# Performance work log

Measured on AMD Instinct MI355X. Metric: run time of the kernel, lower is better.

Reference implementation:

```python
import jax, jax.numpy as jnp
import numpy as np


def setup_inputs() -> dict:
    key = jax.random.key(0)
    k1, k2, k3 = jax.random.split(key, 3)
    B, S, H = 16, 4096, 512           # batch, frames, encoder feature dim
    G, V, D = 2, 320, 128             # groups, codevectors/group, group dim
    return {
        "hidden_states": jax.random.normal(k1, (B, S, H), dtype=jnp.float32),
        "W_proj": jax.random.normal(k2, (H, G * D), dtype=jnp.float32) * 0.02,
        "b_proj": jnp.zeros((G * D,), dtype=jnp.float32),
        "codevectors": jax.random.normal(k3, (G, V, D), dtype=jnp.float32),
    }


def reference(hidden_states, W_proj, b_proj, codevectors):
    B, S, _ = hidden_states.shape
    G, V, D = codevectors.shape
    # project to codevector_dim, split into groups: [B,S,G,D]
    h = (hidden_states @ W_proj + b_proj).reshape(B, S, G, D)
    # squared L2 distances per group, via ||h||^2 - 2 h.c + ||c||^2 -> [G,B,S,V]
    hc = jnp.einsum('bsgd,gvd->gbsv', h, codevectors)
    h2 = jnp.sum(h * h, axis=-1).transpose(2, 0, 1)[..., None]      # [G,B,S,1]
    c2 = jnp.sum(codevectors * codevectors, axis=-1)[:, None, None, :]  # [G,1,1,V]
    distances = h2 - 2.0 * hc + c2                                   # [G,B,S,V]
    indices = jnp.argmin(distances, axis=-1)                         # [G,B,S]
    encodings = jax.nn.one_hot(indices, V, dtype=jnp.float32)        # [G,B,S,V]
    # one-hot matmul gather of selected codevectors, concat groups -> [B,S,G*D]
    quantized_features = jnp.einsum('gbsv,gvd->bsgd', encodings, codevectors).reshape(B, S, G * D)
    # codebook usage perplexity
    avg_probs = jnp.clip(jnp.mean(encodings, axis=(1, 2)), 1e-10, 1.0)  # [G,V]
    perplexity = jnp.mean(jnp.exp(-jnp.sum(avg_probs * jnp.log(avg_probs + 1e-10), axis=-1)))
    return quantized_features, encodings, distances, perplexity
```

## Files before the change

### kernel.cpp

```cpp
#include <hip/hip_runtime.h>
#include <cfloat>

#define M_TOTAL 65536
#define K_H     512
#define GD      256
#define NG      2
#define ND      128
#define NV      320

#define Q_OFF     0
#define ENC_OFF   16777216
#define DIST_OFF  58720256
#define PERP_OFF  100663296

__global__ void c2_kernel(const float* __restrict__ C, float* __restrict__ c2out) {
  int gv = blockIdx.x * 64 + threadIdx.x;
  const float4* p = (const float4*)(C + (size_t)gv * ND);
  float s = 0.f;
#pragma unroll 8
  for (int q = 0; q < 32; ++q) {
    float4 v = p[q];
    s += v.x * v.x + v.y * v.y + v.z * v.z + v.w * v.w;
  }
  c2out[gv] = s;
}

__global__ __launch_bounds__(256, 2) void quant_main(
    const float* __restrict__ X,
    const float* __restrict__ W,
    const float* __restrict__ bias,
    const float* __restrict__ C,
    const float* __restrict__ c2,
    int* __restrict__ hist,
    float* __restrict__ out) {
  __shared__ float hs[64 * 128];
  __shared__ float reg2[8192];

  const int t   = threadIdx.x;
  const int tx  = t & 15;
  const int ty  = t >> 4;
  const int row0 = blockIdx.x * 64;

  float* out_q    = out + Q_OFF;
  float* out_enc  = out + ENC_OFF;
  float* out_dist = out + DIST_OFF;

  for (int g = 0; g < NG; ++g) {
    float acc1[4][8];
#pragma unroll
    for (int i = 0; i < 4; ++i)
#pragma unroll
      for (int j = 0; j < 8; ++j) acc1[i][j] = 0.f;

    for (int kc = 0; kc < 32; ++kc) {
      __syncthreads();
      {
        int r = t >> 2, kq = t & 3;
        float4 x4 = *(const float4*)(X + (size_t)(row0 + r) * K_H + kc * 16 + kq * 4);
        reg2[68 * (4 * kq + 0) + r] = x4.x;
        reg2[68 * (4 * kq + 1) + r] = x4.y;
        reg2[68 * (4 * kq + 2) + r] = x4.z;
        reg2[68 * (4 * kq + 3) + r] = x4.w;
      }
#pragma unroll
      for (int i = 0; i < 2; ++i) {
        int fq = t + 256 * i;
        int k = fq >> 5, c4 = fq & 31;
        float4 w4 = *(const float4*)(W + (size_t)(kc * 16 + k) * GD + g * ND + 4 * c4);
        int c = 4 * c4;
        *(float4*)&reg2[1088 + 160 * k + 20 * (c >> 4) + (c & 15)] = w4;
      }
      __syncthreads();
#pragma unroll
      for (int k = 0; k < 16; ++k) {
        float4 a = *(const float4*)&reg2[68 * k + 4 * ty];
        int wb = 1088 + 160 * k + 20 * (tx >> 1) + 8 * (tx & 1);
        float4 w0 = *(const float4*)&reg2[wb];
        float4 w1 = *(const float4*)&reg2[wb + 4];
        float av[4] = {a.x, a.y, a.z, a.w};
        float wv[8] = {w0.x, w0.y, w0.z, w0.w, w1.x, w1.y, w1.z, w1.w};
#pragma unroll
        for (int i = 0; i < 4; ++i)
#pragma unroll
          for (int j = 0; j < 8; ++j) acc1[i][j] += av[i] * wv[j];
      }
    }
#pragma unroll
    for (int j = 0; j < 8; ++j) {
      float bj = bias[g * ND + 8 * tx + j];
#pragma unroll
      for (int i = 0; i < 4; ++i) acc1[i][j] += bj;
    }
#pragma unroll
    for (int i = 0; i < 4; ++i) {
      int r = 4 * ty + i, sw = r & 7;
      float4 v0 = make_float4(acc1[i][0], acc1[i][1], acc1[i][2], acc1[i][3]);
      float4 v1 = make_float4(acc1[i][4], acc1[i][5], acc1[i][6], acc1[i][7]);
      *(float4*)&hs[128 * r + 4 * ((2 * tx) ^ sw)]     = v0;
      *(float4*)&hs[128 * r + 4 * ((2 * tx + 1) ^ sw)] = v1;
    }
    __syncthreads();

    float h2r[4];
#pragma unroll
    for (int i = 0; i < 4; ++i) {
      int r = 4 * ty + i, sw = r & 7;
      float s = 0.f;
#pragma unroll
      for (int qq = 0; qq < 2; ++qq) {
        int q = tx + 16 * qq;
        float4 v = *(const float4*)&hs[128 * r + 4 * (q ^ sw)];
        s += v.x * v.x + v.y * v.y + v.z * v.z + v.w * v.w;
      }
#pragma unroll
      for (int off = 1; off < 16; off <<= 1) s += __shfl_xor(s, off);
      h2r[i] = s;
    }

    float runval[4]; int runidx[4];
#pragma unroll
    for (int i = 0; i < 4; ++i) { runval[i] = FLT_MAX; runidx[i] = 0; }

    for (int vc = 0; vc < 5; ++vc) {
      int vbase = vc * 64;
      __syncthreads();
#pragma unroll
      for (int i = 0; i < 8; ++i) {
        int fq = t + 256 * i;
        int v = fq >> 5, q = fq & 31;
        float4 cv = *(const float4*)(C + (size_t)((g * NV + vbase + v) * ND) + 4 * q);
        *(float4*)&reg2[128 * v + 4 * (q ^ (v & 7))] = cv;
      }
      __syncthreads();
      float acc[4][4];
#pragma unroll
      for (int i = 0; i < 4; ++i)
#pragma unroll
        for (int j = 0; j < 4; ++j) acc[i][j] = 0.f;
#pragma unroll 4
      for (int q = 0; q < 32; ++q) {
        float4 a[4], b[4];
#pragma unroll
        for (int i = 0; i < 4; ++i) {
          int r = 4 * ty + i;
          a[i] = *(const float4*)&hs[128 * r + 4 * (q ^ (r & 7))];
        }
#pragma unroll
        for (int j = 0; j < 4; ++j) {
          int v = tx + 16 * j;
          b[j] = *(const float4*)&reg2[128 * v + 4 * (q ^ (v & 7))];
        }
#pragma unroll
        for (int i = 0; i < 4; ++i)
#pragma unroll
          for (int j = 0; j < 4; ++j)
            acc[i][j] += a[i].x * b[j].x + a[i].y * b[j].y +
                         a[i].z * b[j].z + a[i].w * b[j].w;
      }
      float c2v[4];
#pragma unroll
      for (int j = 0; j < 4; ++j) c2v[j] = c2[g * NV + vbase + tx + 16 * j];
#pragma unroll
      for (int i = 0; i < 4; ++i) {
        int rg = row0 + 4 * ty + i;
        size_t dbase = (size_t)(g * M_TOTAL + rg) * NV + vbase;
#pragma unroll
        for (int j = 0; j < 4; ++j) {
          float d = h2r[i] - 2.f * acc[i][j] + c2v[j];
          out_dist[dbase + tx + 16 * j] = d;
          int vidx = vbase + tx + 16 * j;
          if (d < runval[i]) { runval[i] = d; runidx[i] = vidx; }
        }
      }
    }

    int fidx[4];
#pragma unroll
    for (int i = 0; i < 4; ++i) {
      float v = runval[i]; int idx = runidx[i];
#pragma unroll
      for (int off = 1; off < 16; off <<= 1) {
        float ov = __shfl_xor(v, off);
        int oi = __shfl_xor(idx, off);
        if (ov < v || (ov == v && oi < idx)) { v = ov; idx = oi; }
      }
      fidx[i] = idx;
      if (tx == 0) {
        int rg = row0 + 4 * ty + i;
        out_enc[(size_t)(g * M_TOTAL + rg) * NV + idx] = 1.0f;
        atomicAdd(&hist[g * NV + idx], 1);
      }
    }
    __syncthreads();
    if (tx == 0) {
#pragma unroll
      for (int i = 0; i < 4; ++i) ((int*)reg2)[4 * ty + i] = fidx[i];
    }
    __syncthreads();
#pragma unroll
    for (int it = 0; it < 8; ++it) {
      int flat = t + 256 * it;
      int r = flat >> 5, q = flat & 31;
      int idx = ((int*)reg2)[r];
      float4 cv = *(const float4*)(C + (size_t)((g * NV + idx) * ND) + 4 * q);
      *(float4*)(out_q + (size_t)(row0 + r) * GD + g * ND + 4 * q) = cv;
    }
  }
}

__global__ void perp_kernel(const int* __restrict__ hist, float* __restrict__ outp) {
  int t = threadIdx.x;
  float s0 = 0.f, s1 = 0.f;
  for (int v = t; v < NV; v += 64) {
    float p0 = fminf(fmaxf((float)hist[v] * (1.0f / 65536.f), 1e-10f), 1.0f);
    float p1 = fminf(fmaxf((float)hist[NV + v] * (1.0f / 65536.f), 1e-10f), 1.0f);
    s0 += p0 * logf(p0 + 1e-10f);
    s1 += p1 * logf(p1 + 1e-10f);
  }
#pragma unroll
  for (int off = 1; off < 64; off <<= 1) {
    s0 += __shfl_xor(s0, off);
    s1 += __shfl_xor(s1, off);
  }
  if (t == 0) outp[0] = 0.5f * (expf(-s0) + expf(-s1));
}

extern "C" void kernel_launch(void* const* d_in, const int* in_sizes, int n_in,
                              void* d_out, int out_size, void* d_ws, size_t ws_size,
                              hipStream_t stream) {
  const float* X    = (const float*)d_in[0];
  const float* W    = (const float*)d_in[1];
  const float* bias = (const float*)d_in[2];
  const float* C    = (const float*)d_in[3];
  float* out = (float*)d_out;

  int*   hist = (int*)d_ws;
  float* c2   = (float*)d_ws + 1024;

  hipMemsetAsync(out + ENC_OFF, 0, (size_t)41943040 * 4, stream);
  hipMemsetAsync(d_ws, 0, 4096, stream);

  c2_kernel<<<10, 64, 0, stream>>>(C, c2);
  quant_main<<<1024, 256, 0, stream>>>(X, W, bias, C, c2, hist, out);
  perp_kernel<<<1, 64, 0, stream>>>(hist, out + PERP_OFF);
}
```

Measured before the change: 1.148 ms.

## Split into projection and distance kernels with register-resident dot products

```diff
diff --git a/kernel.cpp b/kernel.cpp
--- a/kernel.cpp
+++ b/kernel.cpp
@@ -1,210 +1,210 @@
 #include <hip/hip_runtime.h>
 #include <cfloat>
 
-#define M_TOTAL 65536
-#define K_H     512
-#define GD      256
-#define NG      2
-#define ND      128
-#define NV      320
-
-#define Q_OFF     0
-#define ENC_OFF   16777216
-#define DIST_OFF  58720256
-#define PERP_OFF  100663296
-
-__global__ void c2_kernel(const float* __restrict__ C, float* __restrict__ c2out) {
-  int gv = blockIdx.x * 64 + threadIdx.x;
-  const float4* p = (const float4*)(C + (size_t)gv * ND);
-  float s = 0.f;
-#pragma unroll 8
-  for (int q = 0; q < 32; ++q) {
-    float4 v = p[q];
-    s += v.x * v.x + v.y * v.y + v.z * v.z + v.w * v.w;
-  }
-  c2out[gv] = s;
-}
-
-__global__ __launch_bounds__(256, 2) void quant_main(
-    const float* __restrict__ X,
-    const float* __restrict__ W,
-    const float* __restrict__ bias,
-    const float* __restrict__ C,
-    const float* __restrict__ c2,
-    int* __restrict__ hist,
-    float* __restrict__ out) {
-  __shared__ float hs[64 * 128];
-  __shared__ float reg2[8192];
-
-  const int t   = threadIdx.x;
-  const int tx  = t & 15;
-  const int ty  = t >> 4;
-  const int row0 = blockIdx.x * 64;
-
-  float* out_q    = out + Q_OFF;
-  float* out_enc  = out + ENC_OFF;
-  float* out_dist = out + DIST_OFF;
+#define MTOT 65536
+#define KH   512
+#define GD   256
+#define NG   2
+#define ND   128
+#define NV   320
+
+#define Q_OFF    0ull
+#define ENC_OFF  16777216ull
+#define DIST_OFF 58720256ull
+#define PERP_OFF 100663296ull
+
+
+__global__ __launch_bounds__(256) void proj_kernel(
+    const float* __restrict__ X, const float* __restrict__ W,
+    const float* __restrict__ bias, float* __restrict__ hbuf) {
+  __shared__ float h2p[4][64];
+  const int t    = threadIdx.x;
+  const int lane = t & 63;
+  const int wv   = __builtin_amdgcn_readfirstlane(t >> 6);
+  const int col  = (wv << 6) | lane;
+  const int row0 = blockIdx.x << 6;
+
+  float acc[64];
+#pragma unroll
+  for (int r = 0; r < 64; ++r) acc[r] = 0.f;
+
+  for (int kc = 0; kc < 16; ++kc) {
+    float wf[32];
+#pragma unroll
+    for (int k = 0; k < 32; ++k) wf[k] = W[(size_t)(kc * 32 + k) * GD + col];
+    const float* xbase = X + (size_t)row0 * KH + kc * 32;
+    float xa[32], xb[32];
+#pragma unroll
+    for (int k = 0; k < 32; ++k) xa[k] = xbase[k];
+#pragma unroll
+    for (int r = 0; r < 64; r += 2) {
+      const float* nx1 = xbase + (size_t)(r + 1) * KH;
+#pragma unroll
+      for (int k = 0; k < 32; ++k) xb[k] = nx1[k];
+#pragma unroll
+      for (int k = 0; k < 32; ++k) acc[r] = fmaf(xa[k], wf[k], acc[r]);
+      const float* nx2 = xbase + (size_t)(r + 2 < 64 ? r + 2 : r + 1) * KH;
+#pragma unroll
+      for (int k = 0; k < 32; ++k) xa[k] = nx2[k];
+#pragma unroll
+      for (int k = 0; k < 32; ++k) acc[r + 1] = fmaf(xb[k], wf[k], acc[r + 1]);
+    }
+  }
+
+  const float vb = bias[col];
+  float* hrow = hbuf + (size_t)row0 * 320;
+#pragma unroll
+  for (int r = 0; r < 64; ++r) {
+    float h = acc[r] + vb;
+    hrow[(size_t)r * 320 + col] = h;
+    float sq = h * h;
+#pragma unroll
+    for (int off = 1; off < 64; off <<= 1) sq += __shfl_xor(sq, off);
+    if (lane == 0) h2p[wv][r] = sq;
+  }
+  __syncthreads();
+  if (t < 64) {
+    hrow[(size_t)t * 320 + 256] = h2p[0][t] + h2p[1][t];
+    hrow[(size_t)t * 320 + 257] = h2p[2][t] + h2p[3][t];
+  }
+}
+
+__global__ __launch_bounds__(256) void dist_kernel(
+    const float* __restrict__ C, const float* __restrict__ hbuf,
+    float* __restrict__ out, int* __restrict__ hist) {
+  __shared__ float smem[10400];
+  __shared__ float c2l[640];
+  __shared__ float pmin[64][8];
+  __shared__ int   pidx[64][8];
+  __shared__ int   idxbuf[2][64];
+  const int t    = threadIdx.x;
+  const int lane = t & 63;
+  const int wv   = __builtin_amdgcn_readfirstlane(t >> 6);
+  const int row0 = blockIdx.x << 6;
+
+  for (int p = 0; p < 3; ++p) {
+    int gv = t + 256 * p;
+    if (gv < 640) {
+      const float* cp = C + (size_t)gv * ND;
+      float s = 0.f;
+#pragma unroll
+      for (int q = 0; q < 32; ++q) {
+        float4 v = *(const float4*)(cp + 4 * q);
+        s = fmaf(v.x, v.x, s); s = fmaf(v.y, v.y, s);
+        s = fmaf(v.z, v.z, s); s = fmaf(v.w, v.w, s);
+      }
+      c2l[gv] = s;
+    }
+  }
 
   for (int g = 0; g < NG; ++g) {
-    float acc1[4][8];
-#pragma unroll
-    for (int i = 0; i < 4; ++i)
-#pragma unroll
-      for (int j = 0; j < 8; ++j) acc1[i][j] = 0.f;
-
-    for (int kc = 0; kc < 32; ++kc) {
+    __syncthreads();
+#pragma unroll
+    for (int p = 0; p < 8; ++p) {
+      int flat = t + 256 * p;
+      int r = flat >> 5, dq = flat & 31;
+      float4 v = *(const float4*)(hbuf + (size_t)(row0 + r) * 320 + g * ND + 4 * dq);
+      *(float4*)(smem + 132 * r + 4 * dq) = v;
+    }
+    __syncthreads();
+    float hf[128];
+#pragma unroll
+    for (int dq = 0; dq < 32; ++dq)
+      *(float4*)(hf + 4 * dq) = *(const float4*)(smem + 132 * lane + 4 * dq);
+    const float vh2 = hbuf[(size_t)(row0 + lane) * 320 + 256 + g];
+    __syncthreads();
+
+    for (int pass = 0; pass < 2; ++pass) {
+      const int cb = 160 * pass + 40 * wv;
+      const float* cgrp = C + (size_t)g * NV * ND;
+      float ca[32], cbuf[32];
+      {
+        const float* cp0 = cgrp + (size_t)cb * ND;
+#pragma unroll
+        for (int k = 0; k < 32; ++k) ca[k] = cp0[k];
+      }
+      for (int cc = 0; cc < 40; ++cc) {
+        const int colg = cb + cc;
+        const float* cp  = cgrp + (size_t)colg * ND;
+        const float* cpn = cgrp + (size_t)(cc + 1 < 40 ? colg + 1 : colg) * ND;
+        float acc = 0.f;
+#pragma unroll
+        for (int k = 0; k < 32; ++k) cbuf[k] = cp[32 + k];
+#pragma unroll
+        for (int k = 0; k < 32; ++k) acc = fmaf(hf[k], ca[k], acc);
+#pragma unroll
+        for (int k = 0; k < 32; ++k) ca[k] = cp[64 + k];
+#pragma unroll
+        for (int k = 0; k < 32; ++k) acc = fmaf(hf[32 + k], cbuf[k], acc);
+#pragma unroll
+        for (int k = 0; k < 32; ++k) cbuf[k] = cp[96 + k];
+#pragma unroll
+        for (int k = 0; k < 32; ++k) acc = fmaf(hf[64 + k], ca[k], acc);
+#pragma unroll
+        for (int k = 0; k < 32; ++k) ca[k] = cpn[k];
+#pragma unroll
+        for (int k = 0; k < 32; ++k) acc = fmaf(hf[96 + k], cbuf[k], acc);
+        const float c2v = c2l[g * NV + colg];
+        const float d = fmaf(acc, -2.f, vh2 + c2v);
+        smem[65 * (40 * wv + cc) + lane] = d;
+      }
       __syncthreads();
+#pragma unroll
+      for (int q = 0; q < 8; ++q)
+#pragma unroll
+        for (int s = 0; s < 5; ++s) {
+          int row = 8 * q + (t >> 5);
+          int cl  = 32 * s + (t & 31);
+          float d = smem[65 * cl + row];
+          out[DIST_OFF + ((size_t)g * MTOT + row0 + row) * NV + 160 * pass + cl] = d;
+        }
       {
-        int r = t >> 2, kq = t & 3;
-        float4 x4 = *(const float4*)(X + (size_t)(row0 + r) * K_H + kc * 16 + kq * 4);
-        reg2[68 * (4 * kq + 0) + r] = x4.x;
-        reg2[68 * (4 * kq + 1) + r] = x4.y;
-        reg2[68 * (4 * kq + 2) + r] = x4.z;
-        reg2[68 * (4 * kq + 3) + r] = x4.w;
-      }
-#pragma unroll
-      for (int i = 0; i < 2; ++i) {
-        int fq = t + 256 * i;
-        int k = fq >> 5, c4 = fq & 31;
-        float4 w4 = *(const float4*)(W + (size_t)(kc * 16 + k) * GD + g * ND + 4 * c4);
-        int c = 4 * c4;
-        *(float4*)&reg2[1088 + 160 * k + 20 * (c >> 4) + (c & 15)] = w4;
+        int row = t >> 2, part = t & 3;
+        float mv = FLT_MAX; int mi = 0;
+        for (int j = 0; j < 40; ++j) {
+          int cl = part * 40 + j;
+          float d = smem[65 * cl + row];
+          if (d < mv) { mv = d; mi = 160 * pass + cl; }
+        }
+        pmin[row][4 * pass + part] = mv;
+        pidx[row][4 * pass + part] = mi;
       }
       __syncthreads();
-#pragma unroll
-      for (int k = 0; k < 16; ++k) {
-        float4 a = *(const float4*)&reg2[68 * k + 4 * ty];
-        int wb = 1088 + 160 * k + 20 * (tx >> 1) + 8 * (tx & 1);
-        float4 w0 = *(const float4*)&reg2[wb];
-        float4 w1 = *(const float4*)&reg2[wb + 4];
-        float av[4] = {a.x, a.y, a.z, a.w};
-        float wv[8] = {w0.x, w0.y, w0.z, w0.w, w1.x, w1.y, w1.z, w1.w};
-#pragma unroll
-        for (int i = 0; i < 4; ++i)
-#pragma unroll
-          for (int j = 0; j < 8; ++j) acc1[i][j] += av[i] * wv[j];
-      }
-    }
-#pragma unroll
-    for (int j = 0; j < 8; ++j) {
-      float bj = bias[g * ND + 8 * tx + j];
-#pragma unroll
-      for (int i = 0; i < 4; ++i) acc1[i][j] += bj;
-    }
-#pragma unroll
-    for (int i = 0; i < 4; ++i) {
-      int r = 4 * ty + i, sw = r & 7;
-      float4 v0 = make_float4(acc1[i][0], acc1[i][1], acc1[i][2], acc1[i][3]);
-      float4 v1 = make_float4(acc1[i][4], acc1[i][5], acc1[i][6], acc1[i][7]);
-      *(float4*)&hs[128 * r + 4 * ((2 * tx) ^ sw)]     = v0;
-      *(float4*)&hs[128 * r + 4 * ((2 * tx + 1) ^ sw)] = v1;
-    }
-    __syncthreads();
-
-    float h2r[4];
-#pragma unroll
-    for (int i = 0; i < 4; ++i) {
-      int r = 4 * ty + i, sw = r & 7;
-      float s = 0.f;
-#pragma unroll
-      for (int qq = 0; qq < 2; ++qq) {
-        int q = tx + 16 * qq;
-        float4 v = *(const float4*)&hs[128 * r + 4 * (q ^ sw)];
-        s += v.x * v.x + v.y * v.y + v.z * v.z + v.w * v.w;
-      }
-#pragma unroll
-      for (int off = 1; off < 16; off <<= 1) s += __shfl_xor(s, off);
-      h2r[i] = s;
-    }
-
-    float runval[4]; int runidx[4];
-#pragma unroll
-    for (int i = 0; i < 4; ++i) { runval[i] = FLT_MAX; runidx[i] = 0; }
-
-    for (int vc = 0; vc < 5; ++vc) {
-      int vbase = vc * 64;
-      __syncthreads();
-#pragma unroll
-      for (int i = 0; i < 8; ++i) {
-        int fq = t + 256 * i;
-        int v = fq >> 5, q = fq & 31;
-        float4 cv = *(const float4*)(C + (size_t)((g * NV + vbase + v) * ND) + 4 * q);
-        *(float4*)&reg2[128 * v + 4 * (q ^ (v & 7))] = cv;
-      }
-      __syncthreads();
-      float acc[4][4];
-#pragma unroll
-      for (int i = 0; i < 4; ++i)
-#pragma unroll
-        for (int j = 0; j < 4; ++j) acc[i][j] = 0.f;
-#pragma unroll 4
-      for (int q = 0; q < 32; ++q) {
-        float4 a[4], b[4];
-#pragma unroll
-        for (int i = 0; i < 4; ++i) {
-          int r = 4 * ty + i;
-          a[i] = *(const float4*)&hs[128 * r + 4 * (q ^ (r & 7))];
-        }
-#pragma unroll
-        for (int j = 0; j < 4; ++j) {
-          int v = tx + 16 * j;
-          b[j] = *(const float4*)&reg2[128 * v + 4 * (q ^ (v & 7))];
-        }
-#pragma unroll
-        for (int i = 0; i < 4; ++i)
-#pragma unroll
-          for (int j = 0; j < 4; ++j)
-            acc[i][j] += a[i].x * b[j].x + a[i].y * b[j].y +
-                         a[i].z * b[j].z + a[i].w * b[j].w;
-      }
-      float c2v[4];
-#pragma unroll
-      for (int j = 0; j < 4; ++j) c2v[j] = c2[g * NV + vbase + tx + 16 * j];
-#pragma unroll
-      for (int i = 0; i < 4; ++i) {
-        int rg = row0 + 4 * ty + i;
-        size_t dbase = (size_t)(g * M_TOTAL + rg) * NV + vbase;
-#pragma unroll
-        for (int j = 0; j < 4; ++j) {
-          float d = h2r[i] - 2.f * acc[i][j] + c2v[j];
-          out_dist[dbase + tx + 16 * j] = d;
-          int vidx = vbase + tx + 16 * j;
-          if (d < runval[i]) { runval[i] = d; runidx[i] = vidx; }
-        }
-      }
-    }
-
-    int fidx[4];
-#pragma unroll
-    for (int i = 0; i < 4; ++i) {
-      float v = runval[i]; int idx = runidx[i];
-#pragma unroll
-      for (int off = 1; off < 16; off <<= 1) {
-        float ov = __shfl_xor(v, off);
-        int oi = __shfl_xor(idx, off);
-        if (ov < v || (ov == v && oi < idx)) { v = ov; idx = oi; }
-      }
-      fidx[i] = idx;
-      if (tx == 0) {
-        int rg = row0 + 4 * ty + i;
-        out_enc[(size_t)(g * M_TOTAL + rg) * NV + idx] = 1.0f;
-        atomicAdd(&hist[g * NV + idx], 1);
-      }
-    }
-    __syncthreads();
-    if (tx == 0) {
-#pragma unroll
-      for (int i = 0; i < 4; ++i) ((int*)reg2)[4 * ty + i] = fidx[i];
-    }
-    __syncthreads();
-#pragma unroll
-    for (int it = 0; it < 8; ++it) {
-      int flat = t + 256 * it;
-      int r = flat >> 5, q = flat & 31;
-      int idx = ((int*)reg2)[r];
-      float4 cv = *(const float4*)(C + (size_t)((g * NV + idx) * ND) + 4 * q);
-      *(float4*)(out_q + (size_t)(row0 + r) * GD + g * ND + 4 * q) = cv;
-    }
+    }
+    if (t < 64) {
+      float mv = FLT_MAX; int mi = 0;
+#pragma unroll
+      for (int s = 0; s < 8; ++s) {
+        float v = pmin[t][s];
+        if (v < mv) { mv = v; mi = pidx[t][s]; }
+      }
+      idxbuf[g][t] = mi;
+      atomicAdd(&hist[g * NV + mi], 1);
+    }
+  }
+  __syncthreads();
+  for (int g = 0; g < NG; ++g) {
+#pragma unroll
+    for (int q = 0; q < 16; ++q)
+#pragma unroll
+      for (int s = 0; s < 5; ++s) {
+        int row = 4 * q + wv;
+        int col = 64 * s + lane;
+        float v = (col == idxbuf[g][row]) ? 1.f : 0.f;
+        out[ENC_OFF + ((size_t)g * MTOT + row0 + row) * NV + col] = v;
+      }
+  }
+  for (int g = 0; g < NG; ++g) {
+#pragma unroll
+    for (int q = 0; q < 8; ++q)
+#pragma unroll
+      for (int s = 0; s < 4; ++s) {
+        int row = 8 * q + (t >> 5);
+        int d   = 32 * s + (t & 31);
+        int idx = idxbuf[g][row];
+        float v = C[((size_t)g * NV + idx) * ND + d];
+        out[Q_OFF + (size_t)(row0 + row) * GD + g * ND + d] = v;
+      }
   }
 }
 
@@ -233,14 +233,10 @@
   const float* bias = (const float*)d_in[2];
   const float* C    = (const float*)d_in[3];
   float* out = (float*)d_out;
-
-  int*   hist = (int*)d_ws;
-  float* c2   = (float*)d_ws + 1024;
-
-  hipMemsetAsync(out + ENC_OFF, 0, (size_t)41943040 * 4, stream);
-  hipMemsetAsync(d_ws, 0, 4096, stream);
-
-  c2_kernel<<<10, 64, 0, stream>>>(C, c2);
-  quant_main<<<1024, 256, 0, stream>>>(X, W, bias, C, c2, hist, out);
+  int* hist = (int*)d_ws;
+
+  hipMemsetAsync(d_ws, 0, 2560, stream);
+  proj_kernel<<<1024, 256, 0, stream>>>(X, W, bias, out + ENC_OFF);
+  dist_kernel<<<1024, 256, 0, stream>>>(C, out + ENC_OFF, out, hist);
   perp_kernel<<<1, 64, 0, stream>>>(hist, out + PERP_OFF);
 }
```

Measured after the change: 2.718 ms. 137% more time.
